# Optimization experiments

Hardware: AMD Instinct MI355X
Metric: run time of the kernel (lower is better)

Reference implementation:

```python
import jax, jax.numpy as jnp
import numpy as np

RC = 5.0                 # cutoff radius (init kwarg)
B, M = 128, 256          # structures per batch, atoms per structure
L = 17.2                 # box edge (Angstrom) -> ~0.05 atoms/A^3, ~27 nbrs/atom at rc=5
P = 2_097_152            # fixed max pair count (output padding)


def _pairs(coord):
    """Cell-list candidate generation + radius filter, batched over structures.

    Faithful to the TF CellListNL (no 'cell' / open-boundary path): atoms are
    shifted to the positive octant, binned into cells of edge rc, and candidate
    pairs are atoms of the same structure whose cell bins differ by at most 1 in
    every dimension (the 27-cell stencil). Final pairs satisfy 0 < dist < rc.
    """
    pos = coord - jnp.min(coord, axis=0)                          # [N,3] shift (as in TF code)
    cell = jnp.floor(pos / RC).astype(jnp.int32)                  # [N,3] cell bins
    posb = pos.reshape(B, M, 3)
    cellb = cell.reshape(B, M, 3)
    diff = posb[:, None, :, :] - posb[:, :, None, :]              # [B,M,M,3] = pos_j - pos_i
    sq = jnp.sum(diff * diff, axis=-1)                            # [B,M,M]
    nz = sq > 0.0
    dist = jnp.sqrt(jnp.where(nz, sq, 1.0)) * nz                  # safe norm (0 on diagonal)
    # 27-neighbor-cell stencil == per-axis bin difference in {-1,0,1}
    nbr = jnp.all(jnp.abs(cellb[:, None, :, :] - cellb[:, :, None, :]) <= 1, axis=-1)
    mask = nbr & (dist < RC) & nz                                 # [B,M,M]
    return diff, dist, mask


def setup_inputs() -> dict:
    key = jax.random.key(0)
    coord = jax.random.uniform(key, (B * M, 3), jnp.float32) * L  # atoms in [0,L)^3 per structure
    ind_1 = jnp.repeat(jnp.arange(B, dtype=jnp.int32), M)         # structure index per atom
    return {"coord": coord, "ind_1": ind_1}


def reference(coord, ind_1):
    # ind_1 is encoded structurally: atoms are laid out as B contiguous blocks of M,
    # so same-structure pairing is enforced by the batched [B,M,M] computation.
    diff, dist, mask = _pairs(coord)
    b, i, j = jnp.nonzero(mask, size=P, fill_value=0)             # fixed-size pair list
    valid = mask[b, i, j]                                         # False on padded rows
    d = dist[b, i, j] * valid                                     # [P]
    df = diff[b, i, j] * valid[:, None]                           # [P,3]
    ind_2 = jnp.stack([b * M + i, b * M + j], axis=1) * valid[:, None].astype(jnp.int32)
    return ind_2, d, df
```

## Files before the change

kernel.cpp:

```cpp
#include <hip/hip_runtime.h>
#include <float.h>

#define MM 256
#define PP 2097152
#define NBLK 512
#define CBLK 256
#define GTH (NBLK * 256)
#define CAP 1024
#define SQMAX 24.999996185302734375f

typedef unsigned long long u64;


__device__ inline void wave_min3(float& x, float& y, float& z) {
    #pragma unroll
    for (int off = 32; off > 0; off >>= 1) {
        x = fminf(x, __shfl_xor(x, off, 64));
        y = fminf(y, __shfl_xor(y, off, 64));
        z = fminf(z, __shfl_xor(z, off, 64));
    }
}

__device__ inline void zero_range(float* __restrict__ o, int lo, int hi, int g) {
    int a = (lo + 3) & ~3;
    if (a > hi) a = hi;
    if (g < a - lo) o[lo + g] = 0.0f;
    float4* o4 = reinterpret_cast<float4*>(o);
    const float4 z4 = make_float4(0.f, 0.f, 0.f, 0.f);
    for (int q = (a >> 2) + g; q < (hi >> 2); q += GTH) o4[q] = z4;
}

__device__ inline void flush_plane(const float* __restrict__ lds, int n, int pad,
                                   float* __restrict__ gdst, int t) {
    if (n <= 0) return;
    const int end = pad + n;
    const int nb = (end + 3) >> 2;
    for (int m = t; m < nb; m += 256) {
        const int lo = m << 2;
        if (lo >= pad && lo + 4 <= end) {
            *reinterpret_cast<float4*>(gdst + lo) =
                *reinterpret_cast<const float4*>(lds + lo);
        } else {
            const int a = lo < pad ? pad : lo;
            const int bmax = (lo + 4 < end) ? (lo + 4) : end;
            for (int e = a; e < bmax; ++e) gdst[e] = lds[e];
        }
    }
}


__global__ void __launch_bounds__(512)
count_k(const float* __restrict__ coord, float* __restrict__ minvec,
        u64* __restrict__ masks, int* __restrict__ bsums) {
    const int cb = blockIdx.x;
    const int b = cb >> 1, h = cb & 1;
    const int t = threadIdx.x;
    const int lane = t & 63, w = t >> 6;

    __shared__ float4 tile4[4][65];
    __shared__ float lmin[3][8];
    __shared__ int wsum[8];

    const float4* c4 = reinterpret_cast<const float4*>(coord);
    float mx = FLT_MAX, my = FLT_MAX, mz = FLT_MAX;
    #pragma unroll 4
    for (int k = 0; k < 16; ++k) {
        const int basei = (k * 512 + t) * 3;
        const float4 f0 = c4[basei + 0];
        const float4 f1 = c4[basei + 1];
        const float4 f2 = c4[basei + 2];
        mx = fminf(mx, fminf(fminf(f0.x, f0.w), fminf(f1.z, f2.y)));
        my = fminf(my, fminf(fminf(f0.y, f1.x), fminf(f1.w, f2.z)));
        mz = fminf(mz, fminf(fminf(f0.z, f1.y), fminf(f2.x, f2.w)));
    }
    wave_min3(mx, my, mz);
    if (lane == 0) { lmin[0][w] = mx; lmin[1][w] = my; lmin[2][w] = mz; }
    __syncthreads();
    mx = fminf(fminf(fminf(lmin[0][0], lmin[0][1]), fminf(lmin[0][2], lmin[0][3])),
               fminf(fminf(lmin[0][4], lmin[0][5]), fminf(lmin[0][6], lmin[0][7])));
    my = fminf(fminf(fminf(lmin[1][0], lmin[1][1]), fminf(lmin[1][2], lmin[1][3])),
               fminf(fminf(lmin[1][4], lmin[1][5]), fminf(lmin[1][6], lmin[1][7])));
    mz = fminf(fminf(fminf(lmin[2][0], lmin[2][1]), fminf(lmin[2][2], lmin[2][3])),
               fminf(fminf(lmin[2][4], lmin[2][5]), fminf(lmin[2][6], lmin[2][7])));
    if (cb == 0 && t == 0) { minvec[0] = mx; minvec[1] = my; minvec[2] = mz; }

    if (t < 256) {
        const int ja = b * MM + t;
        tile4[t >> 6][t & 63] = make_float4(__fsub_rn(coord[3 * ja + 0], mx),
                                            __fsub_rn(coord[3 * ja + 1], my),
                                            __fsub_rn(coord[3 * ja + 2], mz), 0.0f);
    }
    __syncthreads();

    const int rblk = 2 * h + (t >> 8);
    const int tt = t & 255;
    const int i_loc = tt >> 2, c = tt & 3;
    const float4 pi4 = tile4[rblk][i_loc];
    u64 m = 0ULL;
    for (int jj = 0; jj < 64; ++jj) {
        float4 v = tile4[c][jj];
        float dx = __fsub_rn(v.x, pi4.x);
        float dy = __fsub_rn(v.y, pi4.y);
        float dz = __fsub_rn(v.z, pi4.z);
        float sq = __fadd_rn(__fadd_rn(__fmul_rn(dx, dx), __fmul_rn(dy, dy)),
                             __fmul_rn(dz, dz));
        if (sq > 0.0f && sq <= SQMAX) m |= (1ULL << jj);
    }
    masks[cb * 512 + t] = m;

    int v = __popcll(m);
    #pragma unroll
    for (int off = 32; off > 0; off >>= 1) v += __shfl_xor(v, off, 64);
    if (lane == 0) wsum[w] = v;
    __syncthreads();
    if (t == 0) {
        bsums[cb * 2 + 0] = wsum[0] + wsum[1] + wsum[2] + wsum[3];
        bsums[cb * 2 + 1] = wsum[4] + wsum[5] + wsum[6] + wsum[7];
    }
}

__global__ void __launch_bounds__(256)
write_k(const float* __restrict__ coord, const float* __restrict__ minvec,
        const u64* __restrict__ masks, const int* __restrict__ bsums,
        float* __restrict__ outF) {
    const int t = threadIdx.x;
    const int lane = t & 63, w = t >> 6;

    if (blockIdx.x >= NBLK) {
        __shared__ int sTotZ;
        if (w == 0) {
            int s = 0;
            #pragma unroll
            for (int q = 0; q < 8; ++q) s += bsums[lane * 8 + q];
            #pragma unroll
            for (int off = 32; off > 0; off >>= 1) s += __shfl_xor(s, off, 64);
            if (lane == 0) sTotZ = s;
        }
        __syncthreads();
        const int total = (sTotZ < PP) ? sTotZ : PP;
        const int g = (blockIdx.x - NBLK) * 256 + t;
        zero_range(outF, 2 * total,          2 * PP, g);
        zero_range(outF, 2 * PP + total,     3 * PP, g);
        zero_range(outF, 3 * PP + 3 * total, 6 * PP, g);
        return;
    }

    const int b2 = blockIdx.x;
    const int b = b2 >> 2, rblk = b2 & 3;

    __shared__ float4 tile4[4][65];
    __shared__ int pre[NBLK];
    __shared__ int wsum[4];
    __shared__ __align__(16) float sd[CAP + 4];
    __shared__ __align__(16) float sind[2 * CAP + 4];
    __shared__ __align__(16) float sdf[3 * CAP + 4];

    const float mnx = minvec[0], mny = minvec[1], mnz = minvec[2];
    const int ja = b * MM + t;
    tile4[w][lane] = make_float4(__fsub_rn(coord[3 * ja + 0], mnx),
                                 __fsub_rn(coord[3 * ja + 1], mny),
                                 __fsub_rn(coord[3 * ja + 2], mnz), 0.0f);

    if (w == 0) {
        int v[8]; int s = 0;
        #pragma unroll
        for (int q = 0; q < 8; ++q) { v[q] = bsums[lane * 8 + q]; s += v[q]; }
        int isum = s;
        #pragma unroll
        for (int off = 1; off < 64; off <<= 1) {
            int u = __shfl_up(isum, off, 64);
            if (lane >= off) isum += u;
        }
        int run = isum - s;
        #pragma unroll
        for (int q = 0; q < 8; ++q) { pre[lane * 8 + q] = run; run += v[q]; }
    }
    __syncthreads();
    const int base = pre[b2];

    const u64 mask = masks[b2 * 256 + t];
    const int cnt = __popcll(mask);
    int incl = cnt;
    #pragma unroll
    for (int off = 1; off < 64; off <<= 1) {
        int v = __shfl_up(incl, off, 64);
        if (lane >= off) incl += v;
    }
    if (lane == 63) wsum[w] = incl;
    __syncthreads();
    const int agg = wsum[0] + wsum[1] + wsum[2] + wsum[3];
    int woff = 0;
    for (int k = 0; k < w; ++k) woff += wsum[k];
    const int lexcl = woff + incl - cnt;

    const int i_loc = t >> 2, c = t & 3;
    const float4 pi4 = tile4[rblk][i_loc];
    const int gi = b * MM + rblk * 64 + i_loc;
    const int gj0 = b * MM + c * 64;

    const int nbat = (agg + CAP - 1) / CAP;
    for (int bb = 0; bb < nbat; ++bb) {
        const int wlo = bb * CAP, whi = wlo + CAP;
        const int pbase = base + wlo;
        const int pd = pbase & 3;
        const int pi = (2 * pbase) & 3;
        const int pf = (3 * pbase) & 3;
        int q = lexcl;
        u64 mm = mask;
        while (mm) {
            const int jj = __ffsll((long long)mm) - 1;
            mm &= mm - 1;
            if (q >= whi) break;
            if (q >= wlo) {
                float4 v = tile4[c][jj];
                float dx = __fsub_rn(v.x, pi4.x);
                float dy = __fsub_rn(v.y, pi4.y);
                float dz = __fsub_rn(v.z, pi4.z);
                float sq = __fadd_rn(__fadd_rn(__fmul_rn(dx, dx), __fmul_rn(dy, dy)),
                                     __fmul_rn(dz, dz));
                const int s = q - wlo;
                sd[s + pd] = __fsqrt_rn(sq);
                sind[2 * s + pi + 0] = (float)gi;
                sind[2 * s + pi + 1] = (float)(gj0 + jj);
                sdf[3 * s + pf + 0] = dx;
                sdf[3 * s + pf + 1] = dy;
                sdf[3 * s + pf + 2] = dz;
            }
            q++;
        }
        __syncthreads();
        const int nq = ((agg - wlo) < CAP) ? (agg - wlo) : CAP;
        int rem = PP - pbase; if (rem < 0) rem = 0;
        const int nv = (nq < rem) ? nq : rem;
        flush_plane(sd,   nv,     pd, outF + 2 * PP + pbase - pd,     t);
        flush_plane(sind, 2 * nv, pi, outF + 2 * pbase - pi,          t);
        flush_plane(sdf,  3 * nv, pf, outF + 3 * PP + 3 * pbase - pf, t);
        __syncthreads();
    }
}

extern "C" void kernel_launch(void* const* d_in, const int* in_sizes, int n_in,
                              void* d_out, int out_size, void* d_ws, size_t ws_size,
                              hipStream_t stream) {
    const float* coord = (const float*)d_in[0];
    float* outF = (float*)d_out;

    u64*   masks  = (u64*)d_ws;
    int*   bsums  = (int*)(masks + GTH);
    float* minvec = (float*)(bsums + NBLK);

    count_k<<<CBLK, 512, 0, stream>>>(coord, minvec, masks, bsums);
    write_k<<<2 * NBLK, 256, 0, stream>>>(coord, minvec, masks, bsums, outF);
}
```

Before: 29.29 us.

## Split zero-fill into separate wide kernel and merge count blocks per structure

The count kernel now uses one 1024-thread block per structure instead of two 512-thread blocks, so the global min is reduced by half as many blocks. The padding zero-fill moves out of the write kernel into its own kernel with 2048 blocks, giving more parallelism for the large tail memset. The LDS staging capacity doubles, so emit blocks flush fewer times. The cost is an extra kernel launch and larger LDS use in emit, which may lower occupancy.

```diff
diff --git a/kernel.cpp b/kernel.cpp
--- a/kernel.cpp
+++ b/kernel.cpp
@@ -4,9 +4,10 @@
 #define MM 256
 #define PP 2097152
 #define NBLK 512
-#define CBLK 256
 #define GTH (NBLK * 256)
-#define CAP 1024
+#define ZBLK 2048
+#define ZTH (ZBLK * 256)
+#define CAP 2048
 #define SQMAX 24.999996185302734375f
 
 typedef unsigned long long u64;
@@ -19,15 +20,6 @@
         y = fminf(y, __shfl_xor(y, off, 64));
         z = fminf(z, __shfl_xor(z, off, 64));
     }
-}
-
-__device__ inline void zero_range(float* __restrict__ o, int lo, int hi, int g) {
-    int a = (lo + 3) & ~3;
-    if (a > hi) a = hi;
-    if (g < a - lo) o[lo + g] = 0.0f;
-    float4* o4 = reinterpret_cast<float4*>(o);
-    const float4 z4 = make_float4(0.f, 0.f, 0.f, 0.f);
-    for (int q = (a >> 2) + g; q < (hi >> 2); q += GTH) o4[q] = z4;
 }
 
 __device__ inline void flush_plane(const float* __restrict__ lds, int n, int pad,
@@ -49,23 +41,22 @@
 }
 
 
-__global__ void __launch_bounds__(512)
+__global__ void __launch_bounds__(1024)
 count_k(const float* __restrict__ coord, float* __restrict__ minvec,
         u64* __restrict__ masks, int* __restrict__ bsums) {
-    const int cb = blockIdx.x;
-    const int b = cb >> 1, h = cb & 1;
+    const int b = blockIdx.x;
     const int t = threadIdx.x;
     const int lane = t & 63, w = t >> 6;
 
     __shared__ float4 tile4[4][65];
-    __shared__ float lmin[3][8];
-    __shared__ int wsum[8];
+    __shared__ float lmin[3][16];
+    __shared__ int wsum[16];
 
     const float4* c4 = reinterpret_cast<const float4*>(coord);
     float mx = FLT_MAX, my = FLT_MAX, mz = FLT_MAX;
     #pragma unroll 4
-    for (int k = 0; k < 16; ++k) {
-        const int basei = (k * 512 + t) * 3;
+    for (int k = 0; k < 8; ++k) {
+        const int basei = (k * 1024 + t) * 3;
         const float4 f0 = c4[basei + 0];
         const float4 f1 = c4[basei + 1];
         const float4 f2 = c4[basei + 2];
@@ -76,13 +67,14 @@
     wave_min3(mx, my, mz);
     if (lane == 0) { lmin[0][w] = mx; lmin[1][w] = my; lmin[2][w] = mz; }
     __syncthreads();
-    mx = fminf(fminf(fminf(lmin[0][0], lmin[0][1]), fminf(lmin[0][2], lmin[0][3])),
-               fminf(fminf(lmin[0][4], lmin[0][5]), fminf(lmin[0][6], lmin[0][7])));
-    my = fminf(fminf(fminf(lmin[1][0], lmin[1][1]), fminf(lmin[1][2], lmin[1][3])),
-               fminf(fminf(lmin[1][4], lmin[1][5]), fminf(lmin[1][6], lmin[1][7])));
-    mz = fminf(fminf(fminf(lmin[2][0], lmin[2][1]), fminf(lmin[2][2], lmin[2][3])),
-               fminf(fminf(lmin[2][4], lmin[2][5]), fminf(lmin[2][6], lmin[2][7])));
-    if (cb == 0 && t == 0) { minvec[0] = mx; minvec[1] = my; minvec[2] = mz; }
+    mx = lmin[0][0]; my = lmin[1][0]; mz = lmin[2][0];
+    #pragma unroll
+    for (int q = 1; q < 16; ++q) {
+        mx = fminf(mx, lmin[0][q]);
+        my = fminf(my, lmin[1][q]);
+        mz = fminf(mz, lmin[2][q]);
+    }
+    if (b == 0 && t == 0) { minvec[0] = mx; minvec[1] = my; minvec[2] = mz; }
 
     if (t < 256) {
         const int ja = b * MM + t;
@@ -92,7 +84,7 @@
     }
     __syncthreads();
 
-    const int rblk = 2 * h + (t >> 8);
+    const int rblk = t >> 8;
     const int tt = t & 255;
     const int i_loc = tt >> 2, c = tt & 3;
     const float4 pi4 = tile4[rblk][i_loc];
@@ -106,47 +98,65 @@
                              __fmul_rn(dz, dz));
         if (sq > 0.0f && sq <= SQMAX) m |= (1ULL << jj);
     }
-    masks[cb * 512 + t] = m;
+    masks[b * 1024 + t] = m;
 
     int v = __popcll(m);
     #pragma unroll
     for (int off = 32; off > 0; off >>= 1) v += __shfl_xor(v, off, 64);
     if (lane == 0) wsum[w] = v;
     __syncthreads();
-    if (t == 0) {
-        bsums[cb * 2 + 0] = wsum[0] + wsum[1] + wsum[2] + wsum[3];
-        bsums[cb * 2 + 1] = wsum[4] + wsum[5] + wsum[6] + wsum[7];
-    }
+    if (t < 4)
+        bsums[b * 4 + t] = wsum[4 * t] + wsum[4 * t + 1] +
+                           wsum[4 * t + 2] + wsum[4 * t + 3];
 }
 
 __global__ void __launch_bounds__(256)
-write_k(const float* __restrict__ coord, const float* __restrict__ minvec,
-        const u64* __restrict__ masks, const int* __restrict__ bsums,
-        float* __restrict__ outF) {
+ztail_k(const int* __restrict__ bsums, float* __restrict__ outF) {
     const int t = threadIdx.x;
     const int lane = t & 63, w = t >> 6;
-
-    if (blockIdx.x >= NBLK) {
-        __shared__ int sTotZ;
-        if (w == 0) {
-            int s = 0;
-            #pragma unroll
-            for (int q = 0; q < 8; ++q) s += bsums[lane * 8 + q];
-            #pragma unroll
-            for (int off = 32; off > 0; off >>= 1) s += __shfl_xor(s, off, 64);
-            if (lane == 0) sTotZ = s;
-        }
-        __syncthreads();
-        const int total = (sTotZ < PP) ? sTotZ : PP;
-        const int g = (blockIdx.x - NBLK) * 256 + t;
-        zero_range(outF, 2 * total,          2 * PP, g);
-        zero_range(outF, 2 * PP + total,     3 * PP, g);
-        zero_range(outF, 3 * PP + 3 * total, 6 * PP, g);
-        return;
-    }
-
+    __shared__ int sTot;
+    if (w == 0) {
+        int s = 0;
+        #pragma unroll
+        for (int q = 0; q < 8; ++q) s += bsums[lane * 8 + q];
+        #pragma unroll
+        for (int off = 32; off > 0; off >>= 1) s += __shfl_xor(s, off, 64);
+        if (lane == 0) sTot = s;
+    }
+    __syncthreads();
+    const int total = (sTot < PP) ? sTot : PP;
+    const int g = blockIdx.x * 256 + t;
+    const float4 z4 = make_float4(0.f, 0.f, 0.f, 0.f);
+    float4* o4 = reinterpret_cast<float4*>(outF);
+
+    {
+        const int lo = 2 * total, hi = 2 * PP;
+        int a = (lo + 3) & ~3; if (a > hi) a = hi;
+        if (g < a - lo) outF[lo + g] = 0.0f;
+        for (int q = (a >> 2) + g; q < (hi >> 2); q += ZTH) o4[q] = z4;
+    }
+    {
+        const int lo = 2 * PP + total, hi = 3 * PP;
+        int a = (lo + 3) & ~3; if (a > hi) a = hi;
+        if (g < a - lo) outF[lo + g] = 0.0f;
+        for (int q = (a >> 2) + g; q < (hi >> 2); q += ZTH) o4[q] = z4;
+    }
+    {
+        const int lo = 3 * PP + 3 * total, hi = 6 * PP;
+        int a = (lo + 3) & ~3; if (a > hi) a = hi;
+        if (g < a - lo) outF[lo + g] = 0.0f;
+        for (int q = (a >> 2) + g; q < (hi >> 2); q += ZTH) o4[q] = z4;
+    }
+}
+
+__global__ void __launch_bounds__(256)
+emit_k(const float* __restrict__ coord, const float* __restrict__ minvec,
+       const u64* __restrict__ masks, const int* __restrict__ bsums,
+       float* __restrict__ outF) {
     const int b2 = blockIdx.x;
     const int b = b2 >> 2, rblk = b2 & 3;
+    const int t = threadIdx.x;
+    const int lane = t & 63, w = t >> 6;
 
     __shared__ float4 tile4[4][65];
     __shared__ int pre[NBLK];
@@ -249,6 +259,7 @@
     int*   bsums  = (int*)(masks + GTH);
     float* minvec = (float*)(bsums + NBLK);
 
-    count_k<<<CBLK, 512, 0, stream>>>(coord, minvec, masks, bsums);
-    write_k<<<2 * NBLK, 256, 0, stream>>>(coord, minvec, masks, bsums, outF);
-}
+    count_k<<<128,  1024, 0, stream>>>(coord, minvec, masks, bsums);
+    ztail_k<<<ZBLK, 256,  0, stream>>>(bsums, outF);
+    emit_k <<<NBLK, 256,  0, stream>>>(coord, minvec, masks, bsums, outF);
+}
```

New measurement: 34.09 us. +16.4%, slower.
